# Kernel tuning notes

Measured on AMD Instinct MI355X. Metric: run time of the kernel, lower is better.

The kernel has to match this reference:

```python
import jax, jax.numpy as jnp
import numpy as np

N = 10000       # nodes
E = 320000      # random edges (self-loops added separately)
IN_SIZE = 2
UNITS = 64
B = 32


def setup_inputs() -> dict:
    # --- build normalized Laplacian edges (matches calculate_laplacian) ---
    rng = np.random.default_rng(0)
    rows = np.concatenate([rng.integers(0, N, E), np.arange(N)]).astype(np.int32)
    cols = np.concatenate([rng.integers(0, N, E), np.arange(N)]).astype(np.int32)
    vals = np.ones(E + N, dtype=np.float32)  # A + I entries
    rowsum = np.zeros(N, dtype=np.float64)
    np.add.at(rowsum, rows, vals.astype(np.float64))
    d = np.where(rowsum > 0, rowsum ** -0.5, 0.0).astype(np.float32)
    # normalized_adj: M = D^-1/2 A^T D^-1/2  ->  M[c, r] = d[r]*d[c]*A[r, c]
    m_rows = jnp.asarray(cols, dtype=jnp.int32)
    m_cols = jnp.asarray(rows, dtype=jnp.int32)
    m_vals = jnp.asarray(vals * d[rows] * d[cols])

    key = jax.random.key(0)
    k = jax.random.split(key, 6)
    F = UNITS + IN_SIZE
    stdv1 = 1.0 / np.sqrt(2 * UNITS)
    stdv2 = 1.0 / np.sqrt(UNITS)
    w1 = jax.random.uniform(k[0], (F, 2 * UNITS), jnp.float32, -stdv1, stdv1)
    b1 = jax.random.uniform(k[1], (2 * UNITS,), jnp.float32, -stdv1, stdv1)
    w2 = jax.random.uniform(k[2], (F, UNITS), jnp.float32, -stdv2, stdv2)
    b2 = jax.random.uniform(k[3], (UNITS,), jnp.float32, -stdv2, stdv2)
    inputs = jax.random.normal(k[4], (B, N * IN_SIZE), jnp.float32)
    state = jax.random.normal(k[5], (B, N * UNITS), jnp.float32)
    return {"inputs": inputs, "state": state, "m_rows": m_rows, "m_cols": m_cols,
            "m_vals": m_vals, "w1": w1, "b1": b1, "w2": w2, "b2": b2}


def _gc(inputs, state, m_rows, m_cols, m_vals, w, b, out_size):
    # [B, N, F] with F = in_size + units
    x_s = jnp.concatenate(
        [inputs.reshape(B, N, IN_SIZE), state.reshape(B, N, UNITS)], axis=2)
    f = x_s.shape[2]
    x0 = jnp.transpose(x_s, (1, 2, 0)).reshape(N, f * B)  # einsum ijk->jki, flatten
    # sparse spmm: x1 = M @ x0
    x1 = jax.ops.segment_sum(m_vals[:, None] * x0[m_cols], m_rows, num_segments=N)
    x = jnp.transpose(x1.reshape(N, f, B), (2, 0, 1)).reshape(B * N, f)  # ijk->kij
    x = x @ w + b
    return x.reshape(B, N * out_size)


def reference(inputs, state, m_rows, m_cols, m_vals, w1, b1, w2, b2):
    value = jax.nn.sigmoid(_gc(inputs, state, m_rows, m_cols, m_vals, w1, b1, 2 * UNITS))
    # NOTE: faithful to original: split of FLATTENED [B, N*2U] at the midpoint
    r, u = jnp.split(value, 2, axis=1)
    c = jax.nn.relu(_gc(inputs, r * state, m_rows, m_cols, m_vals, w2, b2, UNITS))
    new_h = u * state + (1.0 - u) * c
    return new_h
```

## Files before the change

kernel.cpp:

```cpp
#include <hip/hip_runtime.h>
#include <hip/hip_fp16.h>
#include <cstdint>
#include <cstdio>

#define N_NODES 10000
#define BATCH   32
#define UNITS   64
#define F_DIM   66
#define XROW    2048
#define KPAD    96
#define ASTR    104
#define GRP     10

typedef float v2f __attribute__((ext_vector_type(2)));
typedef float f32x4 __attribute__((ext_vector_type(4)));
typedef _Float16 half8 __attribute__((ext_vector_type(8)));

__device__ __forceinline__ float sigmoidf(float x) {
  return 1.0f / (1.0f + __expf(-x));
}

__global__ __launch_bounds__(256) void hist_k(const int* __restrict__ rows,
                                              int* __restrict__ counts, int E2,
                                              const float* __restrict__ w1,
                                              const float* __restrict__ w2,
                                              _Float16* __restrict__ w1T,
                                              _Float16* __restrict__ w2T) {
  int e = blockIdx.x * 256 + threadIdx.x;
  if (e < E2) atomicAdd(&counts[rows[e]], 1);
  if (e < 128 * KPAD) {
    int j = e / KPAD, f = e % KPAD;
    w1T[e] = (f < 66) ? (_Float16)w1[f * 128 + j] : (_Float16)0.0f;
  } else if (e < 128 * KPAD + 64 * KPAD) {
    int k = e - 128 * KPAD;
    int j = k / KPAD, f = k % KPAD;
    w2T[k] = (f < 66) ? (_Float16)w2[f * 64 + j] : (_Float16)0.0f;
  }
}

__global__ __launch_bounds__(256) void scan_k(const int* __restrict__ counts,
                                              int* __restrict__ rowptr,
                                              int* __restrict__ wofs, int n) {
  __shared__ int lbuf[10240];
  __shared__ int sums[256];
  int t = threadIdx.x;
  for (int i = t; i < N_NODES / 4; i += 256)
    reinterpret_cast<int4*>(lbuf)[i] = reinterpret_cast<const int4*>(counts)[i];
  for (int i = N_NODES + t; i < 10240; i += 256) lbuf[i] = 0;
  __syncthreads();
  int base = t * 40;
  int v[40];
  int run = 0;
#pragma unroll
  for (int i = 0; i < 40; ++i) { v[i] = run; run += lbuf[base + i]; }
  sums[t] = run;
  __syncthreads();
  for (int off = 1; off < 256; off <<= 1) {
    int x = (t >= off) ? sums[t - off] : 0;
    __syncthreads();
    sums[t] += x;
    __syncthreads();
  }
  int tbase = (t == 0) ? 0 : sums[t - 1];
#pragma unroll
  for (int i = 0; i < 40; ++i) lbuf[base + i] = tbase + v[i];
  __syncthreads();
  for (int i = t; i < N_NODES / 4; i += 256) {
    int4 w = reinterpret_cast<int4*>(lbuf)[i];
    reinterpret_cast<int4*>(rowptr)[i] = w;
    reinterpret_cast<int4*>(wofs)[i] = w;
  }
  if (t == 255) rowptr[N_NODES] = sums[255];
}

__device__ __forceinline__ void pack_row_fp8(const float* T, int n, int t,
                                             unsigned char* xcat8) {
  int k0 = t * 8;
  int f8 = k0 >> 5;
  int b0 = k0 & 31;
  const float* Ts = &T[(f8 + 2) * 33 + b0];
  int d0 = __builtin_amdgcn_cvt_pk_fp8_f32(Ts[0], Ts[1], 0, false);
  d0     = __builtin_amdgcn_cvt_pk_fp8_f32(Ts[2], Ts[3], d0, true);
  int d1 = __builtin_amdgcn_cvt_pk_fp8_f32(Ts[4], Ts[5], 0, false);
  d1     = __builtin_amdgcn_cvt_pk_fp8_f32(Ts[6], Ts[7], d1, true);
  *reinterpret_cast<uint2*>(xcat8 + (size_t)n * XROW + k0) = make_uint2(d0, d1);
}

__global__ __launch_bounds__(256) void scat_build(const int* __restrict__ rows,
                                                  const int* __restrict__ cols,
                                                  const float* __restrict__ vals,
                                                  int* __restrict__ wofs,
                                                  int2* __restrict__ ecv, int E2,
                                                  const float* __restrict__ inputs,
                                                  const float* __restrict__ state,
                                                  unsigned char* __restrict__ xcat8,
                                                  __half2* __restrict__ xin) {
  int blk = blockIdx.x, t = threadIdx.x;
  if (blk >= N_NODES) {
    int e = (blk - N_NODES) * 256 + t;
    if (e < E2) {
      int r = rows[e];
      int p = atomicAdd(&wofs[r], 1);
      ecv[p] = make_int2(cols[e] << 11, __float_as_int(vals[e]));
    }
    return;
  }
  int n = blk;
  __shared__ float T[66 * 33];
  int f = t & 63, bq = t >> 6;
#pragma unroll
  for (int bb = 0; bb < 8; ++bb) {
    int b = bq + bb * 4;
    T[(f + 2) * 33 + b] = state[(size_t)b * 640000 + (size_t)n * 64 + f];
  }
  if (t < 64) {
    int b0 = t & 31, f0 = t >> 5;
    T[f0 * 33 + b0] = inputs[(size_t)b0 * 20000 + (size_t)n * 2 + f0];
  }
  __syncthreads();
  pack_row_fp8(T, n, t, xcat8);
  if (t < 32) {
    int f0 = t >> 4, b = (t & 15) * 2;
    xin[(size_t)n * 32 + t] = __floats2half2_rn(T[f0 * 33 + b], T[f0 * 33 + b + 1]);
  }
}

__global__ __launch_bounds__(256) void yin_k(const int* __restrict__ rowptr,
                                             const int2* __restrict__ ecv,
                                             const __half* __restrict__ xin,
                                             float* __restrict__ yin) {
  int n = blockIdx.x * 32 + (threadIdx.x >> 3);
  int lane = threadIdx.x & 7;
  if (n >= N_NODES) return;
  float acc[8];
#pragma unroll
  for (int i = 0; i < 8; ++i) acc[i] = 0.0f;
  int s = rowptr[n], e = rowptr[n + 1];
  for (int ee = s; ee < e; ++ee) {
    int2 cv = ecv[ee];
    float v = __int_as_float(cv.y);
    const char* p = reinterpret_cast<const char*>(xin) + (size_t)((unsigned)cv.x >> 4);
    uint4 raw = reinterpret_cast<const uint4*>(p)[lane];
    const __half2* h = reinterpret_cast<const __half2*>(&raw);
#pragma unroll
    for (int i = 0; i < 4; ++i) {
      float2 x = __half22float2(h[i]);
      acc[2 * i]     += v * x.x;
      acc[2 * i + 1] += v * x.y;
    }
  }
  float4* dst = reinterpret_cast<float4*>(yin + (size_t)n * 64 + lane * 8);
  dst[0] = make_float4(acc[0], acc[1], acc[2], acc[3]);
  dst[1] = make_float4(acc[4], acc[5], acc[6], acc[7]);
}

__device__ __forceinline__ void consume8f8(uint2 u, float v, v2f* acc) {
  v2f p0 = __builtin_amdgcn_cvt_pk_f32_fp8((int)u.x, false);
  v2f p1 = __builtin_amdgcn_cvt_pk_f32_fp8((int)u.x, true);
  v2f p2 = __builtin_amdgcn_cvt_pk_f32_fp8((int)u.y, false);
  v2f p3 = __builtin_amdgcn_cvt_pk_f32_fp8((int)u.y, true);
  v2f vv = {v, v};
  acc[0] += vv * p0;
  acc[1] += vv * p1;
  acc[2] += vv * p2;
  acc[3] += vv * p3;
}

__device__ __forceinline__ void ld_grp(const int2* __restrict__ ep, int gsz,
                                       const unsigned char* __restrict__ xcat8,
                                       unsigned t8, uint2* r, float* v) {
#pragma unroll
  for (int q = 0; q < GRP; ++q) {
    int2 c = ep[q];
    if (q >= gsz) { c.x = 0; c.y = 0; }
    unsigned off = (unsigned)c.x + t8;
    r[q] = *reinterpret_cast<const uint2*>(xcat8 + off);
    v[q] = __int_as_float(c.y);
  }
}

__device__ __forceinline__ void cons_grp(const uint2* r, const float* v, v2f* acc) {
#pragma unroll
  for (int q = 0; q < GRP; ++q) consume8f8(r[q], v[q], acc);
}

__device__ __forceinline__ void spmm_body(int n, int t,
                                          const int* __restrict__ rowptr,
                                          const int2* __restrict__ ecv,
                                          const unsigned char* __restrict__ xcat8,
                                          const float* __restrict__ yin,
                                          _Float16* accH) {
  v2f acc[4];
#pragma unroll
  for (int i = 0; i < 4; ++i) acc[i] = (v2f){0.0f, 0.0f};

  unsigned t8 = (unsigned)t * 8u;
  int s = rowptr[n], e = rowptr[n + 1];
  int ne = e - s;
  int ng = (ne + GRP - 1) / GRP;
  const int2* ep = ecv + s;

  uint2 rA[GRP], rB[GRP];
  float vA[GRP], vB[GRP];
  ld_grp(ep, ne, xcat8, t8, rA, vA);
  int g = 1;
  for (; g + 1 < ng; g += 2) {
    ld_grp(ep + GRP * g, ne - GRP * g, xcat8, t8, rB, vB);
    cons_grp(rA, vA, acc);
    ld_grp(ep + GRP * (g + 1), ne - GRP * (g + 1), xcat8, t8, rA, vA);
    cons_grp(rB, vB, acc);
  }
  if (g < ng) {
    ld_grp(ep + GRP * g, ne - GRP * g, xcat8, t8, rB, vB);
    cons_grp(rA, vA, acc);
    cons_grp(rB, vB, acc);
  } else {
    cons_grp(rA, vA, acc);
  }

  {
    int f8 = t >> 2;
    int b0 = (t & 3) * 8;
    float a[8] = {acc[0].x, acc[0].y, acc[1].x, acc[1].y,
                  acc[2].x, acc[2].y, acc[3].x, acc[3].y};
    _Float16* dst = accH + (f8 + 2);
#pragma unroll
    for (int i = 0; i < 8; ++i) {
      dst[(b0 + i) * ASTR] = (_Float16)a[i];
    }
  }
  if (t < 64) {
    int f = t >> 5, b = t & 31;
    accH[b * ASTR + f] = (_Float16)yin[(size_t)n * 64 + t];
  }
  for (int id = t; id < 32 * 19; id += 256) {
    int b = id / 19, c = id % 19;
    *reinterpret_cast<unsigned int*>(
        reinterpret_cast<char*>(accH) + b * (ASTR * 2) + 132 + c * 4) = 0u;
  }
  __syncthreads();
}

__global__ __launch_bounds__(256) void gcn1(const int* __restrict__ rowptr,
                                            const int2* __restrict__ ecv,
                                            const unsigned char* __restrict__ xcat8,
                                            const float* __restrict__ yin,
                                            const _Float16* __restrict__ w1T,
                                            const float* __restrict__ b1,
                                            const float* __restrict__ state,
                                            unsigned char* __restrict__ xcat2,
                                            __half* __restrict__ valu) {
  int n = blockIdx.x, t = threadIdx.x;
  __shared__ _Float16 accH[32 * ASTR];
  __shared__ __align__(16) char regionA[32 * 136 * 2];

  spmm_body(n, t, rowptr, ecv, xcat8, yin, accH);

  int wv = t >> 6, l = t & 63;
  int mt = wv & 1, ntb = (wv >> 1) * 4;
  int lr = l & 15, lg = l >> 4;
  const _Float16* aB = accH + (size_t)(mt * 16 + lr) * ASTR + lg * 8;
  half8 afr0 = *reinterpret_cast<const half8*>(aB);
  half8 afr1 = *reinterpret_cast<const half8*>(aB + 32);
  half8 afr2 = *reinterpret_cast<const half8*>(aB + 64);
  _Float16* vstage = reinterpret_cast<_Float16*>(regionA);

#pragma unroll
  for (int tt = 0; tt < 4; ++tt) {
    int j = (ntb + tt) * 16 + lr;
    const _Float16* wB = w1T + (size_t)j * KPAD + lg * 8;
    f32x4 c = {0.0f, 0.0f, 0.0f, 0.0f};
    c = __builtin_amdgcn_mfma_f32_16x16x32_f16(afr0, *reinterpret_cast<const half8*>(wB), c, 0, 0, 0);
    c = __builtin_amdgcn_mfma_f32_16x16x32_f16(afr1, *reinterpret_cast<const half8*>(wB + 32), c, 0, 0, 0);
    c = __builtin_amdgcn_mfma_f32_16x16x32_f16(afr2, *reinterpret_cast<const half8*>(wB + 64), c, 0, 0, 0);
    float bj = b1[j];
#pragma unroll
    for (int i = 0; i < 4; ++i) {
      int b = mt * 16 + lg * 4 + i;
      vstage[b * 136 + j] = (_Float16)sigmoidf(c[i] + bj);
    }
  }
  __syncthreads();

  if (n < 5000) {
    int nn_i = t >> 7;
    int f    = t & 63;
    int bg   = (t >> 6) & 1;
    int nn = n * 2 + nn_i;
    int jj = nn_i * 64 + f;
    const float* sp = state + (size_t)nn * 64 + f;
    const _Float16* vp = vstage + jj;
    int bbase = bg * 16;
    unsigned int d[4];
#pragma unroll
    for (int q = 0; q < 4; ++q) {
      int b0 = bbase + q * 4;
      float x0 = (float)vp[(b0 + 0) * 136] * sp[(size_t)(b0 + 0) * 640000];
      float x1 = (float)vp[(b0 + 1) * 136] * sp[(size_t)(b0 + 1) * 640000];
      float x2 = (float)vp[(b0 + 2) * 136] * sp[(size_t)(b0 + 2) * 640000];
      float x3 = (float)vp[(b0 + 3) * 136] * sp[(size_t)(b0 + 3) * 640000];
      int dd = __builtin_amdgcn_cvt_pk_fp8_f32(x0, x1, 0, false);
      dd     = __builtin_amdgcn_cvt_pk_fp8_f32(x2, x3, dd, true);
      d[q] = (unsigned)dd;
    }
    *reinterpret_cast<uint4*>(xcat2 + (size_t)nn * XROW + f * 32 + bbase) =
        make_uint4(d[0], d[1], d[2], d[3]);
  } else {
    int b = t >> 3, jg = t & 7;
    const uint4* src = reinterpret_cast<const uint4*>(vstage + b * 136 + jg * 16);
    uint4 q0 = src[0];
    uint4 q1 = src[1];
    __half* vb = valu + (size_t)(n - 5000) * 4096 + b * 128 + jg * 16;
    *reinterpret_cast<uint4*>(vb) = q0;
    *reinterpret_cast<uint4*>(vb + 8) = q1;
  }
}

__global__ __launch_bounds__(256) void gcn2(const int* __restrict__ rowptr,
                                            const int2* __restrict__ ecv,
                                            const unsigned char* __restrict__ xcat2,
                                            const float* __restrict__ yin,
                                            const _Float16* __restrict__ w2T,
                                            const float* __restrict__ b2,
                                            const __half* __restrict__ valu,
                                            const float* __restrict__ state,
                                            float* __restrict__ out) {
  int n = blockIdx.x, t = threadIdx.x;
  __shared__ _Float16 accH[32 * ASTR];
  __shared__ __align__(16) char regionA[32 * 68 * 4];

  spmm_body(n, t, rowptr, ecv, xcat2, yin, accH);

  int wv = t >> 6, l = t & 63;
  int mt = wv & 1, ntb = (wv >> 1) * 2;
  int lr = l & 15, lg = l >> 4;
  const _Float16* aB = accH + (size_t)(mt * 16 + lr) * ASTR + lg * 8;
  half8 afr0 = *reinterpret_cast<const half8*>(aB);
  half8 afr1 = *reinterpret_cast<const half8*>(aB + 32);
  half8 afr2 = *reinterpret_cast<const half8*>(aB + 64);
  float* ostage = reinterpret_cast<float*>(regionA);

#pragma unroll
  for (int tt = 0; tt < 2; ++tt) {
    int j = (ntb + tt) * 16 + lr;
    const _Float16* wB = w2T + (size_t)j * KPAD + lg * 8;
    f32x4 c = {0.0f, 0.0f, 0.0f, 0.0f};
    c = __builtin_amdgcn_mfma_f32_16x16x32_f16(afr0, *reinterpret_cast<const half8*>(wB), c, 0, 0, 0);
    c = __builtin_amdgcn_mfma_f32_16x16x32_f16(afr1, *reinterpret_cast<const half8*>(wB + 32), c, 0, 0, 0);
    c = __builtin_amdgcn_mfma_f32_16x16x32_f16(afr2, *reinterpret_cast<const half8*>(wB + 64), c, 0, 0, 0);
    float bj = b2[j];
#pragma unroll
    for (int i = 0; i < 4; ++i) {
      int b = mt * 16 + lg * 4 + i;
      ostage[b * 68 + j] = fmaxf(c[i] + bj, 0.0f);
    }
  }
  __syncthreads();

  int bg = t >> 4, jg = t & 15;
  int n2 = n >> 1, no = n & 1;
  const __half* up = valu + (size_t)n2 * 4096 + (size_t)no * 64 + jg * 4;
#pragma unroll
  for (int i = 0; i < 2; ++i) {
    int b = bg * 2 + i;
    size_t idx = (size_t)b * 640000 + (size_t)n * 64 + jg * 4;
    float4 sv = *reinterpret_cast<const float4*>(state + idx);
    float4 cc = *reinterpret_cast<const float4*>(ostage + b * 68 + jg * 4);
    union { uint2 u; __half2 h[2]; } pk;
    pk.u = *reinterpret_cast<const uint2*>(up + (size_t)b * 128);
    float2 u01 = __half22float2(pk.h[0]);
    float2 u23 = __half22float2(pk.h[1]);
    float4 h;
    h.x = u01.x * sv.x + (1.0f - u01.x) * cc.x;
    h.y = u01.y * sv.y + (1.0f - u01.y) * cc.y;
    h.z = u23.x * sv.z + (1.0f - u23.x) * cc.z;
    h.w = u23.y * sv.w + (1.0f - u23.y) * cc.w;
    *reinterpret_cast<float4*>(out + idx) = h;
  }
}

static inline size_t alignup(size_t x) { return (x + 255) & ~(size_t)255; }

extern "C" void kernel_launch(void* const* d_in, const int* in_sizes, int n_in,
                              void* d_out, int out_size, void* d_ws, size_t ws_size,
                              hipStream_t stream) {
  const float* inputs = (const float*)d_in[0];
  const float* state  = (const float*)d_in[1];
  const int*   m_rows = (const int*)d_in[2];
  const int*   m_cols = (const int*)d_in[3];
  const float* m_vals = (const float*)d_in[4];
  const float* w1     = (const float*)d_in[5];
  const float* b1     = (const float*)d_in[6];
  const float* w2     = (const float*)d_in[7];
  const float* b2     = (const float*)d_in[8];
  float* out = (float*)d_out;

  const int N  = N_NODES;
  const int E2 = in_sizes[2];

  char* ws = (char*)d_ws;
  size_t off = 0;
  int* counts = (int*)(ws + off); off = alignup(off + (size_t)N * 4);
  int* rowptr = (int*)(ws + off); off = alignup(off + (size_t)(N + 1) * 4);
  int* wofs   = (int*)(ws + off); off = alignup(off + (size_t)N * 4);
  int2* ecv   = (int2*)(ws + off); off = alignup(off + (size_t)E2 * 8 + 256);
  unsigned char* xcat8 = (unsigned char*)(ws + off); off = alignup(off + (size_t)N * XROW);
  unsigned char* xcat2 = (unsigned char*)(ws + off); off = alignup(off + (size_t)N * XROW);
  __half* valu = (__half*)(ws + off); off = alignup(off + (size_t)5000 * 4096 * 2);
  float* yin  = (float*)(ws + off); off = alignup(off + (size_t)N * 64 * 4);
  __half* xin = (__half*)(ws + off); off = alignup(off + (size_t)N * 64 * 2);
  _Float16* w1T = (_Float16*)(ws + off); off = alignup(off + (size_t)128 * KPAD * 2);
  _Float16* w2T = (_Float16*)(ws + off); off = alignup(off + (size_t)64 * KPAD * 2);
  if (off > ws_size) { return; }

  hipMemsetAsync(counts, 0, (size_t)N * 4, stream);

  int eb = (E2 + 255) / 256;
  hipLaunchKernelGGL(hist_k,     dim3(eb), dim3(256), 0, stream, m_rows, counts, E2,
                     w1, w2, w1T, w2T);
  hipLaunchKernelGGL(scan_k,     dim3(1),  dim3(256), 0, stream, counts, rowptr, wofs, N);
  hipLaunchKernelGGL(scat_build, dim3(N + eb), dim3(256), 0, stream,
                     m_rows, m_cols, m_vals, wofs, ecv, E2,
                     inputs, state, xcat8, (__half2*)xin);
  hipLaunchKernelGGL(yin_k,      dim3((N + 31) / 32), dim3(256), 0, stream,
                     rowptr, ecv, xin, yin);
  hipLaunchKernelGGL(gcn1,       dim3(N),  dim3(256), 0, stream, rowptr, ecv,
                     xcat8, yin, w1T, b1, state, xcat2, valu);
  hipLaunchKernelGGL(gcn2,       dim3(N),  dim3(256), 0, stream, rowptr, ecv,
                     xcat2, yin, w2T, b2, valu, state, out);
}
```

Measured before the change: 437.6 us.

## Alias shared buffers, raise occupancy hints, and parallelize yin SpMM across edges

The gcn1/gcn2 kernels now reuse one shared-memory buffer for both the SpMM accumulator and the output staging area, with an extra barrier between the two uses. They also declare launch bounds of 8 blocks per SM, so more blocks can be resident at once. The yin kernel moves from 8 lanes per node to a full wavefront per node that splits edges across 4 slots and reduces them with shuffles. The edge group size drops from 10 to 8. The lower footprint may raise occupancy for the latency-bound gathers, at the cost of an extra sync and possible register spills.

```diff
diff --git a/kernel.cpp b/kernel.cpp
--- a/kernel.cpp
+++ b/kernel.cpp
@@ -10,7 +10,7 @@
 #define XROW    2048
 #define KPAD    96
 #define ASTR    104
-#define GRP     10
+#define GRP     8
 
 typedef float v2f __attribute__((ext_vector_type(2)));
 typedef float f32x4 __attribute__((ext_vector_type(4)));
@@ -129,29 +129,39 @@
                                              const int2* __restrict__ ecv,
                                              const __half* __restrict__ xin,
                                              float* __restrict__ yin) {
-  int n = blockIdx.x * 32 + (threadIdx.x >> 3);
-  int lane = threadIdx.x & 7;
+  int n = (blockIdx.x * 256 + threadIdx.x) >> 6;
   if (n >= N_NODES) return;
-  float acc[8];
-#pragma unroll
-  for (int i = 0; i < 8; ++i) acc[i] = 0.0f;
+  int lane  = threadIdx.x & 63;
+  int eslot = lane >> 4;
+  int sub   = lane & 15;
+  unsigned sb = (unsigned)sub * 8u;
+
+  float acc0 = 0.0f, acc1 = 0.0f, acc2 = 0.0f, acc3 = 0.0f;
   int s = rowptr[n], e = rowptr[n + 1];
-  for (int ee = s; ee < e; ++ee) {
+  const char* xb = reinterpret_cast<const char*>(xin);
+  for (int ee = s + eslot; ee < e; ee += 4) {
     int2 cv = ecv[ee];
     float v = __int_as_float(cv.y);
-    const char* p = reinterpret_cast<const char*>(xin) + (size_t)((unsigned)cv.x >> 4);
-    uint4 raw = reinterpret_cast<const uint4*>(p)[lane];
-    const __half2* h = reinterpret_cast<const __half2*>(&raw);
-#pragma unroll
-    for (int i = 0; i < 4; ++i) {
-      float2 x = __half22float2(h[i]);
-      acc[2 * i]     += v * x.x;
-      acc[2 * i + 1] += v * x.y;
-    }
-  }
-  float4* dst = reinterpret_cast<float4*>(yin + (size_t)n * 64 + lane * 8);
-  dst[0] = make_float4(acc[0], acc[1], acc[2], acc[3]);
-  dst[1] = make_float4(acc[4], acc[5], acc[6], acc[7]);
+    unsigned off = ((unsigned)cv.x >> 4) + sb;
+    uint2 raw = *reinterpret_cast<const uint2*>(xb + off);
+    __half2 h0 = *reinterpret_cast<__half2*>(&raw.x);
+    __half2 h1 = *reinterpret_cast<__half2*>(&raw.y);
+    float2 x0 = __half22float2(h0);
+    float2 x1 = __half22float2(h1);
+    acc0 += v * x0.x; acc1 += v * x0.y;
+    acc2 += v * x1.x; acc3 += v * x1.y;
+  }
+#pragma unroll
+  for (int m = 16; m <= 32; m <<= 1) {
+    acc0 += __shfl_xor(acc0, m);
+    acc1 += __shfl_xor(acc1, m);
+    acc2 += __shfl_xor(acc2, m);
+    acc3 += __shfl_xor(acc3, m);
+  }
+  if (eslot == 0) {
+    *reinterpret_cast<float4*>(yin + (size_t)n * 64 + sub * 4) =
+        make_float4(acc0, acc1, acc2, acc3);
+  }
 }
 
 __device__ __forceinline__ void consume8f8(uint2 u, float v, v2f* acc) {
@@ -241,18 +251,18 @@
   __syncthreads();
 }
 
-__global__ __launch_bounds__(256) void gcn1(const int* __restrict__ rowptr,
-                                            const int2* __restrict__ ecv,
-                                            const unsigned char* __restrict__ xcat8,
-                                            const float* __restrict__ yin,
-                                            const _Float16* __restrict__ w1T,
-                                            const float* __restrict__ b1,
-                                            const float* __restrict__ state,
-                                            unsigned char* __restrict__ xcat2,
-                                            __half* __restrict__ valu) {
+__global__ __launch_bounds__(256, 8) void gcn1(const int* __restrict__ rowptr,
+                                               const int2* __restrict__ ecv,
+                                               const unsigned char* __restrict__ xcat8,
+                                               const float* __restrict__ yin,
+                                               const _Float16* __restrict__ w1T,
+                                               const float* __restrict__ b1,
+                                               const float* __restrict__ state,
+                                               unsigned char* __restrict__ xcat2,
+                                               __half* __restrict__ valu) {
   int n = blockIdx.x, t = threadIdx.x;
-  __shared__ _Float16 accH[32 * ASTR];
-  __shared__ __align__(16) char regionA[32 * 136 * 2];
+  __shared__ __align__(16) char smem[32 * 136 * 2];
+  _Float16* accH = reinterpret_cast<_Float16*>(smem);
 
   spmm_body(n, t, rowptr, ecv, xcat8, yin, accH);
 
@@ -263,7 +273,8 @@
   half8 afr0 = *reinterpret_cast<const half8*>(aB);
   half8 afr1 = *reinterpret_cast<const half8*>(aB + 32);
   half8 afr2 = *reinterpret_cast<const half8*>(aB + 64);
-  _Float16* vstage = reinterpret_cast<_Float16*>(regionA);
+  __syncthreads();
+  _Float16* vstage = reinterpret_cast<_Float16*>(smem);
 
 #pragma unroll
   for (int tt = 0; tt < 4; ++tt) {
@@ -316,18 +327,18 @@
   }
 }
 
-__global__ __launch_bounds__(256) void gcn2(const int* __restrict__ rowptr,
-                                            const int2* __restrict__ ecv,
-                                            const unsigned char* __restrict__ xcat2,
-                                            const float* __restrict__ yin,
-                                            const _Float16* __restrict__ w2T,
-                                            const float* __restrict__ b2,
-                                            const __half* __restrict__ valu,
-                                            const float* __restrict__ state,
-                                            float* __restrict__ out) {
+__global__ __launch_bounds__(256, 8) void gcn2(const int* __restrict__ rowptr,
+                                               const int2* __restrict__ ecv,
+                                               const unsigned char* __restrict__ xcat2,
+                                               const float* __restrict__ yin,
+                                               const _Float16* __restrict__ w2T,
+                                               const float* __restrict__ b2,
+                                               const __half* __restrict__ valu,
+                                               const float* __restrict__ state,
+                                               float* __restrict__ out) {
   int n = blockIdx.x, t = threadIdx.x;
-  __shared__ _Float16 accH[32 * ASTR];
-  __shared__ __align__(16) char regionA[32 * 68 * 4];
+  __shared__ __align__(16) char smem[32 * 68 * 4];
+  _Float16* accH = reinterpret_cast<_Float16*>(smem);
 
   spmm_body(n, t, rowptr, ecv, xcat2, yin, accH);
 
@@ -338,7 +349,8 @@
   half8 afr0 = *reinterpret_cast<const half8*>(aB);
   half8 afr1 = *reinterpret_cast<const half8*>(aB + 32);
   half8 afr2 = *reinterpret_cast<const half8*>(aB + 64);
-  float* ostage = reinterpret_cast<float*>(regionA);
+  __syncthreads();
+  float* ostage = reinterpret_cast<float*>(smem);
 
 #pragma unroll
   for (int tt = 0; tt < 2; ++tt) {
@@ -422,7 +434,7 @@
   hipLaunchKernelGGL(scat_build, dim3(N + eb), dim3(256), 0, stream,
                      m_rows, m_cols, m_vals, wofs, ecv, E2,
                      inputs, state, xcat8, (__half2*)xin);
-  hipLaunchKernelGGL(yin_k,      dim3((N + 31) / 32), dim3(256), 0, stream,
+  hipLaunchKernelGGL(yin_k,      dim3((N + 3) / 4), dim3(256), 0, stream,
                      rowptr, ecv, xin, yin);
   hipLaunchKernelGGL(gcn1,       dim3(N),  dim3(256), 0, stream, rowptr, ecv,
                      xcat8, yin, w1T, b1, state, xcat2, valu);
```

Result: slower. 508.5 us (+16.2%).
